# Optimization experiments

Measured on AMD Instinct MI355X. Metric: run time of the kernel, lower is better.

The kernel has to match this reference:

```python
import jax, jax.numpy as jnp
from jax import lax
import numpy as np

T, B, I, U = 512, 64, 512, 512
FORGET_BIAS = 1.0  # matches forget_bias=1.0; cell_clip=None -> no clipping; no peephole


def setup_inputs() -> dict:
    key = jax.random.key(0)
    kx, kw = jax.random.split(key)
    x = jax.random.normal(kx, (T, B, I), dtype=jnp.float32)
    cs0 = jnp.zeros((B, U), dtype=jnp.float32)
    h0 = jnp.zeros((B, U), dtype=jnp.float32)
    # kernel [input_size + num_units, 4*num_units], bias [4*num_units] (zeros init as in build())
    w = jax.random.normal(kw, (I + U, 4 * U), dtype=jnp.float32) * 0.05
    b = jnp.zeros((4 * U,), dtype=jnp.float32)
    return {"x": x, "cs0": cs0, "h0": h0, "w": w, "b": b}


def reference(x, cs0, h0, w, b):
    """Fused BlockLSTM forward. Returns (h_seq [T,B,U], final_cs, final_h),
    mirroring LSTMBlockWrapper.call -> (outputs, (cell_state, output))."""

    def step(carry, x_t):
        cs_prev, h_prev = carry
        z = jnp.concatenate([x_t, h_prev], axis=-1) @ w + b  # [B, 4U]
        # TF BlockLSTM gate order: i, ci (cell input), f, o
        zi, zci, zf, zo = jnp.split(z, 4, axis=-1)
        i = jax.nn.sigmoid(zi)
        f = jax.nn.sigmoid(zf + FORGET_BIAS)
        ci = jnp.tanh(zci)
        cs = ci * i + cs_prev * f  # no cell_clip (cell_clip=-1)
        h = jnp.tanh(cs) * jax.nn.sigmoid(zo)
        return (cs, h), h

    (final_cs, final_h), h_seq = lax.scan(step, (cs0, h0), x)
    return h_seq, final_cs, final_h
```

## Files before the change

kernel.cpp:

```cpp
#include <hip/hip_runtime.h>


#define T_STEPS 512
#define NB 64
#define NU 512
#define NI 512
#define KTOT 1024
#define ZCOLS 2048
#define HSEQ_ELEMS (T_STEPS * NB * NU)
#define POISON64 0x7FC07FC07FC07FC0ull
#define SLEEP_PRE 10

typedef float    floatx4   __attribute__((ext_vector_type(4)));
typedef __bf16   bf16x8    __attribute__((ext_vector_type(8)));
typedef unsigned short ushortx8 __attribute__((ext_vector_type(8)));
typedef unsigned long long ull_t;

static __device__ __forceinline__ unsigned short f2bf(float f) {
  unsigned int u = __builtin_bit_cast(unsigned int, f);
  u += 0x7fffu + ((u >> 16) & 1u);
  return (unsigned short)(u >> 16);
}
static __device__ __forceinline__ float bf2f(unsigned short h) {
  unsigned int u = ((unsigned int)h) << 16;
  return __builtin_bit_cast(float, u);
}
static __device__ __forceinline__ float sigmoidf_(float x) {
  return __builtin_amdgcn_rcpf(1.0f + __expf(-x));
}
static __device__ __forceinline__ float fast_tanhf(float x) {
  const float ax = fabsf(x);
  const float t = __expf(-2.0f * ax);
  const float r = (1.0f - t) * __builtin_amdgcn_rcpf(1.0f + t);
  return copysignf(r, x);
}
static __device__ __forceinline__ bf16x8 ldfrag(const unsigned short* p) {
  ushortx8 v = *reinterpret_cast<const ushortx8*>(p);
  return __builtin_bit_cast(bf16x8, v);
}
static __device__ __forceinline__ ull_t pack4bf(float a, float b, float c, float d) {
  return (ull_t)f2bf(a) | ((ull_t)f2bf(b) << 16) | ((ull_t)f2bf(c) << 32) |
         ((ull_t)f2bf(d) << 48);
}
static __device__ __forceinline__ bf16x8 mkfrag(ull_t lo, ull_t hi) {
  struct P { ull_t a, b; } s{lo, hi};
  return __builtin_bit_cast(bf16x8, s);
}

__global__ __launch_bounds__(256) void init_kernel(const float* __restrict__ h0,
                                                   unsigned short* __restrict__ hbf) {
  const int j = blockIdx.x * 256 + threadIdx.x;
  if (j < 524288) {
    ull_t* p = reinterpret_cast<ull_t*>(&hbf[32768 + (size_t)j * 32]);
#pragma unroll
    for (int r = 0; r < 8; ++r) p[r] = POISON64;
  } else {
    const int k = j - 524288;
#pragma unroll
    for (int p2 = 0; p2 < 2; ++p2) {
      const int i = k * 2 + p2;
      const int row = i >> 6, chunk = i & 63;
      const float* src = &h0[row * NU + chunk * 8];
      const ull_t lo = pack4bf(src[0], src[4], src[1], src[5]);
      const ull_t hi = pack4bf(src[2], src[6], src[3], src[7]);
      const size_t off =
          (size_t)(chunk >> 2) * 2048 + (size_t)(chunk & 3) * 512 + (size_t)row * 8;
      *reinterpret_cast<ull_t*>(&hbf[off]) = lo;
      *reinterpret_cast<ull_t*>(&hbf[off + 4]) = hi;
    }
  }
}

__global__ __launch_bounds__(256) void transpose_w_kernel(
    const float* __restrict__ w, unsigned short* __restrict__ wT) {
  __shared__ float tile[32][33];
  const int u0 = blockIdx.x * 32;
  const int k0 = blockIdx.y * 32;
  const int g = blockIdx.z;
  const int tx = threadIdx.x & 31, ty = threadIdx.x >> 5;
#pragma unroll
  for (int r = 0; r < 4; ++r) {
    const int k = ty + r * 8;
    tile[k][tx] = w[(size_t)(k0 + k) * ZCOLS + g * 512 + u0 + tx];
  }
  __syncthreads();
#pragma unroll
  for (int r = 0; r < 4; ++r) {
    const int u = ty + r * 8;
    const int kk = k0 + tx;
    int kd = kk;
    if (kk >= 512) {
      const int u3 = kk & 7;
      kd = (kk & ~7) | (((u3 & 3) << 1) | (u3 >> 2));
    }
    wT[(size_t)((u0 + u) * 4 + g) * KTOT + kd] = f2bf(tile[tx][u]);
  }
}

__global__ __launch_bounds__(256) void gemm_zx_kernel(
    const float* __restrict__ x, const unsigned short* __restrict__ wT,
    const float* __restrict__ bias, unsigned short* __restrict__ zxp) {
  __shared__ __align__(16) unsigned short As[128][32];
  __shared__ __align__(16) unsigned short Bs[128][32];
  const int m0 = blockIdx.y * 128;
  const int n0 = blockIdx.x * 128;
  const int tid = threadIdx.x;
  const int wid = tid >> 6, lane = tid & 63;
  const int quad = lane >> 4, nl = lane & 15;
  const int wm = (wid & 1) * 64, wn = (wid >> 1) * 64;
  const int srow = tid >> 3;
  const int skk = (tid & 7) * 4;

  floatx4 acc[4][4] = {};

  for (int kt = 0; kt < 16; ++kt) {
    const int k0 = kt * 32;
    __syncthreads();
#pragma unroll
    for (int r = 0; r < 4; ++r) {
      const int row = r * 32 + srow;
      const float4 v =
          *reinterpret_cast<const float4*>(&x[(size_t)(m0 + row) * NI + k0 + skk]);
      *reinterpret_cast<ull_t*>(&As[row][skk]) = pack4bf(v.x, v.y, v.z, v.w);
      *reinterpret_cast<ull_t*>(&Bs[row][skk]) =
          *reinterpret_cast<const ull_t*>(&wT[(size_t)(n0 + row) * KTOT + k0 + skk]);
    }
    __syncthreads();
    bf16x8 af[4], bfr[4];
#pragma unroll
    for (int i = 0; i < 4; ++i) {
      af[i] = ldfrag(&As[wm + i * 16 + nl][quad * 8]);
      bfr[i] = ldfrag(&Bs[wn + i * 16 + nl][quad * 8]);
    }
#pragma unroll
    for (int i = 0; i < 4; ++i)
#pragma unroll
      for (int j = 0; j < 4; ++j)
        acc[i][j] =
            __builtin_amdgcn_mfma_f32_16x16x32_bf16(af[i], bfr[j], acc[i][j], 0, 0, 0);
  }

  float bv[4];
#pragma unroll
  for (int j = 0; j < 4; ++j) {
    const int colp = n0 + wn + j * 16 + nl;
    bv[j] = bias[(colp & 3) * 512 + (colp >> 2)];
  }
#pragma unroll
  for (int i = 0; i < 4; ++i) {
    const int browb = wm + i * 16 + quad * 4;
    const int t = (m0 + browb) >> 6;
    const int rt = (browb >> 5) & 1;
    const int hi = (browb & 31) >> 3;
    const int qb = (browb >> 2) & 1;
#pragma unroll
    for (int j = 0; j < 4; ++j) {
      const int colp = n0 + wn + j * 16 + nl;
      const int cbl = colp >> 5;
      const int lanep = (colp & 31) + 32 * qb;
      const ull_t packed =
          pack4bf(acc[i][j][0] + bv[j], acc[i][j][1] + bv[j],
                  acc[i][j][2] + bv[j], acc[i][j][3] + bv[j]);
      *reinterpret_cast<ull_t*>(
          &zxp[((((size_t)t * 64 + cbl) * 2 + rt) * 64 + lanep) * 16 + hi * 4]) = packed;
    }
  }
}

__global__ __launch_bounds__(64) void lstm_rec_kernel(
    const unsigned short* __restrict__ zxp, const unsigned short* __restrict__ wT,
    const float* __restrict__ cs_init, float* __restrict__ out,
    unsigned short* __restrict__ hbf) {
  const int lane = threadIdx.x;
  const int bid = blockIdx.x;
  const int cb = bid >> 2;
  const int qr = bid & 3;
  const int l15 = lane & 15, quad = lane >> 4;
  const int row = qr * 16 + l15;

  bf16x8 Wf[2][16];
#pragma unroll
  for (int cf = 0; cf < 2; ++cf)
#pragma unroll
    for (int kf = 0; kf < 16; ++kf)
      Wf[cf][kf] = ldfrag(
          &wT[(size_t)(cb * 32 + cf * 16 + l15) * KTOT + 512 + kf * 32 + quad * 8]);

  float csv[2];
  csv[0] = cs_init[row * NU + cb * 8 + quad];
  csv[1] = cs_init[row * NU + cb * 8 + 4 + quad];

  ull_t AL[16], AH[16];
  auto issueA = [&](int tt) {
    const unsigned short* p0 =
        hbf + (size_t)tt * 32768 + (size_t)quad * 512 + (size_t)row * 8;
#pragma unroll
    for (int kf = 0; kf < 16; ++kf) {
      const unsigned short* p = p0 + (size_t)kf * 2048;
      AL[kf] = __hip_atomic_load((const ull_t*)p, __ATOMIC_RELAXED,
                                 __HIP_MEMORY_SCOPE_AGENT);
      AH[kf] = __hip_atomic_load((const ull_t*)(p + 4), __ATOMIC_RELAXED,
                                 __HIP_MEMORY_SCOPE_AGENT);
    }
  };

  unsigned short zxv[8];
  const int rt_ = qr >> 1;
  const int qb_ = (l15 >> 2) & 1;
  const int hi_ = (qr & 1) * 2 + (l15 >> 3);
  const int rr_ = l15 & 3;
  auto issueZ = [&](int tt) {
    const size_t base = (((size_t)tt * 64 + cb) * 2 + rt_) * 64;
#pragma unroll
    for (int cf = 0; cf < 2; ++cf)
#pragma unroll
      for (int g = 0; g < 4; ++g) {
        const int c5 = cf * 16 + quad * 4 + g;
        zxv[cf * 4 + g] = zxp[(base + (size_t)(c5 + 32 * qb_)) * 16 + hi_ * 4 + rr_];
      }
  };

  issueA(0);
  issueZ(0);

  for (int t = 0; t < T_STEPS; ++t) {
    floatx4 z0, z1;
    int tries = 0;
    while (true) {
      floatx4 p00 = {0.f, 0.f, 0.f, 0.f}, p01 = {0.f, 0.f, 0.f, 0.f};
      floatx4 p10 = {0.f, 0.f, 0.f, 0.f}, p11 = {0.f, 0.f, 0.f, 0.f};
#pragma unroll
      for (int kf = 0; kf < 8; ++kf) {
        const bf16x8 hlo = mkfrag(AL[kf], AH[kf]);
        const bf16x8 hhi = mkfrag(AL[8 + kf], AH[8 + kf]);
        p00 = __builtin_amdgcn_mfma_f32_16x16x32_bf16(Wf[0][kf], hlo, p00, 0, 0, 0);
        p01 = __builtin_amdgcn_mfma_f32_16x16x32_bf16(Wf[1][kf], hlo, p01, 0, 0, 0);
        p10 = __builtin_amdgcn_mfma_f32_16x16x32_bf16(Wf[0][8 + kf], hhi, p10, 0, 0, 0);
        p11 = __builtin_amdgcn_mfma_f32_16x16x32_bf16(Wf[1][8 + kf], hhi, p11, 0, 0, 0);
      }
      z0 = p00 + p10;
      z1 = p01 + p11;
      const float s = ((z0[0] + z0[1]) + (z0[2] + z0[3])) +
                      ((z1[0] + z1[1]) + (z1[2] + z1[3]));
      if (!__any(s != s) || ++tries >= (1 << 16)) break;
      issueA(t);
    }

    float hout[2];
    {
      const float iv = sigmoidf_(z0[0] + bf2f(zxv[0]));
      const float civ = fast_tanhf(z0[1] + bf2f(zxv[1]));
      const float fv = sigmoidf_(z0[2] + bf2f(zxv[2]) + 1.0f);
      const float ov = sigmoidf_(z0[3] + bf2f(zxv[3]));
      csv[0] = civ * iv + csv[0] * fv;
      hout[0] = fast_tanhf(csv[0]) * ov;
    }
    {
      const float iv = sigmoidf_(z1[0] + bf2f(zxv[4]));
      const float civ = fast_tanhf(z1[1] + bf2f(zxv[5]));
      const float fv = sigmoidf_(z1[2] + bf2f(zxv[6]) + 1.0f);
      const float ov = sigmoidf_(z1[3] + bf2f(zxv[7]));
      csv[1] = civ * iv + csv[1] * fv;
      hout[1] = fast_tanhf(csv[1]) * ov;
    }

    const unsigned hv = (unsigned)f2bf(hout[0]) | ((unsigned)f2bf(hout[1]) << 16);
    unsigned short* hw = &hbf[(size_t)(t + 1) * 32768 + (size_t)(cb >> 2) * 2048 +
                              (size_t)(cb & 3) * 512 + (size_t)row * 8 + 2 * quad];
    __hip_atomic_store(reinterpret_cast<unsigned*>(hw), hv, __ATOMIC_RELAXED,
                       __HIP_MEMORY_SCOPE_AGENT);
    asm volatile("" ::: "memory");

    float* op = &out[((size_t)t * NB + row) * NU + cb * 8];
    op[quad] = hout[0];
    op[4 + quad] = hout[1];
    if (t == T_STEPS - 1) {
      float* cp = &out[HSEQ_ELEMS + (size_t)row * NU + cb * 8];
      cp[quad] = csv[0];
      cp[4 + quad] = csv[1];
      float* hp2 = &out[HSEQ_ELEMS + NB * NU + (size_t)row * NU + cb * 8];
      hp2[quad] = hout[0];
      hp2[4 + quad] = hout[1];
    }

    if (t + 1 < T_STEPS) {
      __builtin_amdgcn_s_sleep(SLEEP_PRE);
      asm volatile("" ::: "memory");
      issueA(t + 1);
      issueZ(t + 1);
    }
  }
}

extern "C" void kernel_launch(void* const* d_in, const int* in_sizes, int n_in,
                              void* d_out, int out_size, void* d_ws, size_t ws_size,
                              hipStream_t stream) {
  const float* x = (const float*)d_in[0];
  const float* cs0 = (const float*)d_in[1];
  const float* h0 = (const float*)d_in[2];
  const float* w = (const float*)d_in[3];
  const float* bias = (const float*)d_in[4];
  float* out = (float*)d_out;

  char* ws = (char*)d_ws;
  unsigned short* wT = (unsigned short*)(ws);
  unsigned short* zxp = (unsigned short*)(ws + (size_t)(4 << 20));
  unsigned short* hbf = (unsigned short*)(ws + (size_t)(132 << 20));

  init_kernel<<<dim3(2056), 256, 0, stream>>>(h0, hbf);
  transpose_w_kernel<<<dim3(16, 32, 4), 256, 0, stream>>>(w, wT);
  gemm_zx_kernel<<<dim3(16, 256), 256, 0, stream>>>(x, wT, bias, zxp);
  lstm_rec_kernel<<<dim3(256), 64, 0, stream>>>(zxp, wT, cs0, out, hbf);
}
```

Baseline: 1.315 ms.

## Partition recurrent LSTM by XCD with per-XCD batch groups and coherence-tuned polling

The persistent recurrent kernel now assigns work by XCD. Each workgroup reads its hardware XCC id and claims a slot from a per-XCD atomic counter, so every 8-row batch group is handled entirely within one XCD. Extra workgroups exit early. The h buffer layout is reorganised per 8-row group, so polling loads can use non-agent-scope (L2-local) dwordx4 loads, with a fallback to system-coherent loads when a group is not native or keeps retrying. It also removes the fixed sleep, double-buffers the zx prefetch, and overlaps the zx load with compute. The risks are that half the MFMA rows are wasted, the kernel relies on XCD placement from launching 1024 blocks, and correctness depends on cache coherence behaviour.

```diff
diff --git a/kernel.cpp b/kernel.cpp
--- a/kernel.cpp
+++ b/kernel.cpp
@@ -9,7 +9,6 @@
 #define ZCOLS 2048
 #define HSEQ_ELEMS (T_STEPS * NB * NU)
 #define POISON64 0x7FC07FC07FC07FC0ull
-#define SLEEP_PRE 10
 
 typedef float    floatx4   __attribute__((ext_vector_type(4)));
 typedef __bf16   bf16x8    __attribute__((ext_vector_type(8)));
@@ -42,13 +41,11 @@
   return (ull_t)f2bf(a) | ((ull_t)f2bf(b) << 16) | ((ull_t)f2bf(c) << 32) |
          ((ull_t)f2bf(d) << 48);
 }
-static __device__ __forceinline__ bf16x8 mkfrag(ull_t lo, ull_t hi) {
-  struct P { ull_t a, b; } s{lo, hi};
-  return __builtin_bit_cast(bf16x8, s);
-}
 
 __global__ __launch_bounds__(256) void init_kernel(const float* __restrict__ h0,
-                                                   unsigned short* __restrict__ hbf) {
+                                                   unsigned short* __restrict__ hbf,
+                                                   unsigned int* __restrict__ qcnt) {
+  if (blockIdx.x == 0 && threadIdx.x < 8) qcnt[threadIdx.x * 64] = 0;
   const int j = blockIdx.x * 256 + threadIdx.x;
   if (j < 524288) {
     ull_t* p = reinterpret_cast<ull_t*>(&hbf[32768 + (size_t)j * 32]);
@@ -59,12 +56,12 @@
 #pragma unroll
     for (int p2 = 0; p2 < 2; ++p2) {
       const int i = k * 2 + p2;
-      const int row = i >> 6, chunk = i & 63;
-      const float* src = &h0[row * NU + chunk * 8];
+      const int row = i >> 6, cb = i & 63;
+      const float* src = &h0[row * NU + cb * 8];
       const ull_t lo = pack4bf(src[0], src[4], src[1], src[5]);
       const ull_t hi = pack4bf(src[2], src[6], src[3], src[7]);
-      const size_t off =
-          (size_t)(chunk >> 2) * 2048 + (size_t)(chunk & 3) * 512 + (size_t)row * 8;
+      const size_t off = (size_t)(row >> 3) * 4096 + (size_t)(cb >> 2) * 256 +
+                         (size_t)(cb & 3) * 64 + (size_t)(row & 7) * 8;
       *reinterpret_cast<ull_t*>(&hbf[off]) = lo;
       *reinterpret_cast<ull_t*>(&hbf[off + 4]) = hi;
     }
@@ -170,13 +167,26 @@
 __global__ __launch_bounds__(64) void lstm_rec_kernel(
     const unsigned short* __restrict__ zxp, const unsigned short* __restrict__ wT,
     const float* __restrict__ cs_init, float* __restrict__ out,
-    unsigned short* __restrict__ hbf) {
+    unsigned short* __restrict__ hbf, unsigned int* __restrict__ qcnt) {
   const int lane = threadIdx.x;
-  const int bid = blockIdx.x;
-  const int cb = bid >> 2;
-  const int qr = bid & 3;
+
+  unsigned xcd;
+  asm volatile("s_getreg_b32 %0, hwreg(HW_REG_XCC_ID)" : "=s"(xcd));
+  xcd &= 7;
+  int g = -1, cb = -1;
+  bool native = false;
+  for (int q = 0; q < 8; ++q) {
+    const int qq = (int)((xcd + q) & 7);
+    int s = 0;
+    if (lane == 0) s = (int)atomicAdd(&qcnt[qq * 64], 1u);
+    s = __shfl(s, 0);
+    if (s < 64) { g = qq; cb = s; native = (q == 0); break; }
+  }
+  if (g < 0) return;
+
   const int l15 = lane & 15, quad = lane >> 4;
-  const int row = qr * 16 + l15;
+  const int r8 = l15 & 7;
+  const int row = g * 8 + r8;
 
   bf16x8 Wf[2][16];
 #pragma unroll
@@ -190,49 +200,59 @@
   csv[0] = cs_init[row * NU + cb * 8 + quad];
   csv[1] = cs_init[row * NU + cb * 8 + 4 + quad];
 
-  ull_t AL[16], AH[16];
-  auto issueA = [&](int tt) {
+  floatx4 Af[16];
+  auto issueA = [&](int tt, bool ag) {
     const unsigned short* p0 =
-        hbf + (size_t)tt * 32768 + (size_t)quad * 512 + (size_t)row * 8;
-#pragma unroll
-    for (int kf = 0; kf < 16; ++kf) {
-      const unsigned short* p = p0 + (size_t)kf * 2048;
-      AL[kf] = __hip_atomic_load((const ull_t*)p, __ATOMIC_RELAXED,
-                                 __HIP_MEMORY_SCOPE_AGENT);
-      AH[kf] = __hip_atomic_load((const ull_t*)(p + 4), __ATOMIC_RELAXED,
-                                 __HIP_MEMORY_SCOPE_AGENT);
+        hbf + (size_t)tt * 32768 + (size_t)g * 4096 + quad * 64 + r8 * 8;
+    if (ag) {
+#pragma unroll
+      for (int kf = 0; kf < 16; ++kf)
+        asm volatile("global_load_dwordx4 %0, %1, off sc0 sc1"
+                     : "=v"(Af[kf]) : "v"(p0 + (size_t)kf * 256) : "memory");
+    } else {
+#pragma unroll
+      for (int kf = 0; kf < 16; ++kf)
+        asm volatile("global_load_dwordx4 %0, %1, off sc0"
+                     : "=v"(Af[kf]) : "v"(p0 + (size_t)kf * 256) : "memory");
     }
   };
 
-  unsigned short zxv[8];
-  const int rt_ = qr >> 1;
-  const int qb_ = (l15 >> 2) & 1;
-  const int hi_ = (qr & 1) * 2 + (l15 >> 3);
-  const int rr_ = l15 & 3;
-  auto issueZ = [&](int tt) {
+  const int rt_ = row >> 5;
+  const int qb_ = (row >> 2) & 1;
+  const int hi_ = (row & 31) >> 3;
+  const int rr_ = row & 3;
+  auto issueZ = [&](int tt, unsigned short (&zb)[8]) {
     const size_t base = (((size_t)tt * 64 + cb) * 2 + rt_) * 64;
 #pragma unroll
     for (int cf = 0; cf < 2; ++cf)
 #pragma unroll
-      for (int g = 0; g < 4; ++g) {
-        const int c5 = cf * 16 + quad * 4 + g;
-        zxv[cf * 4 + g] = zxp[(base + (size_t)(c5 + 32 * qb_)) * 16 + hi_ * 4 + rr_];
+      for (int gg = 0; gg < 4; ++gg) {
+        const int c5 = cf * 16 + quad * 4 + gg;
+        zb[cf * 4 + gg] = zxp[(base + (size_t)(c5 + 32 * qb_)) * 16 + hi_ * 4 + rr_];
       }
   };
 
-  issueA(0);
-  issueZ(0);
-
-  for (int t = 0; t < T_STEPS; ++t) {
+  unsigned short zA[8], zB[8];
+  bool agent = !native;
+  int astreak = 0;
+
+  issueA(0, agent);
+  issueZ(0, zA);
+  asm volatile("" ::: "memory");
+
+  auto step = [&](int t, unsigned short (&zrd)[8], unsigned short (&zwr)[8]) {
     floatx4 z0, z1;
     int tries = 0;
-    while (true) {
+    bool sa = agent;
+    for (;;) {
+      asm volatile("s_waitcnt vmcnt(0)" ::: "memory");
+      __builtin_amdgcn_sched_barrier(0);
       floatx4 p00 = {0.f, 0.f, 0.f, 0.f}, p01 = {0.f, 0.f, 0.f, 0.f};
       floatx4 p10 = {0.f, 0.f, 0.f, 0.f}, p11 = {0.f, 0.f, 0.f, 0.f};
 #pragma unroll
       for (int kf = 0; kf < 8; ++kf) {
-        const bf16x8 hlo = mkfrag(AL[kf], AH[kf]);
-        const bf16x8 hhi = mkfrag(AL[8 + kf], AH[8 + kf]);
+        const bf16x8 hlo = __builtin_bit_cast(bf16x8, Af[kf]);
+        const bf16x8 hhi = __builtin_bit_cast(bf16x8, Af[8 + kf]);
         p00 = __builtin_amdgcn_mfma_f32_16x16x32_bf16(Wf[0][kf], hlo, p00, 0, 0, 0);
         p01 = __builtin_amdgcn_mfma_f32_16x16x32_bf16(Wf[1][kf], hlo, p01, 0, 0, 0);
         p10 = __builtin_amdgcn_mfma_f32_16x16x32_bf16(Wf[0][8 + kf], hhi, p10, 0, 0, 0);
@@ -243,52 +263,66 @@
       const float s = ((z0[0] + z0[1]) + (z0[2] + z0[3])) +
                       ((z1[0] + z1[1]) + (z1[2] + z1[3]));
       if (!__any(s != s) || ++tries >= (1 << 16)) break;
-      issueA(t);
-    }
+      if (!sa && tries >= 8) sa = true;
+      issueA(t, sa);
+    }
+    if (!agent) {
+      if (sa) { if (++astreak >= 16) agent = true; }
+      else astreak = 0;
+    }
+
+    if (t + 1 < T_STEPS) issueZ(t + 1, zwr);
+    asm volatile("" ::: "memory");
 
     float hout[2];
     {
-      const float iv = sigmoidf_(z0[0] + bf2f(zxv[0]));
-      const float civ = fast_tanhf(z0[1] + bf2f(zxv[1]));
-      const float fv = sigmoidf_(z0[2] + bf2f(zxv[2]) + 1.0f);
-      const float ov = sigmoidf_(z0[3] + bf2f(zxv[3]));
+      const float iv = sigmoidf_(z0[0] + bf2f(zrd[0]));
+      const float civ = fast_tanhf(z0[1] + bf2f(zrd[1]));
+      const float fv = sigmoidf_(z0[2] + bf2f(zrd[2]) + 1.0f);
+      const float ov = sigmoidf_(z0[3] + bf2f(zrd[3]));
       csv[0] = civ * iv + csv[0] * fv;
       hout[0] = fast_tanhf(csv[0]) * ov;
     }
     {
-      const float iv = sigmoidf_(z1[0] + bf2f(zxv[4]));
-      const float civ = fast_tanhf(z1[1] + bf2f(zxv[5]));
-      const float fv = sigmoidf_(z1[2] + bf2f(zxv[6]) + 1.0f);
-      const float ov = sigmoidf_(z1[3] + bf2f(zxv[7]));
+      const float iv = sigmoidf_(z1[0] + bf2f(zrd[4]));
+      const float civ = fast_tanhf(z1[1] + bf2f(zrd[5]));
+      const float fv = sigmoidf_(z1[2] + bf2f(zrd[6]) + 1.0f);
+      const float ov = sigmoidf_(z1[3] + bf2f(zrd[7]));
       csv[1] = civ * iv + csv[1] * fv;
       hout[1] = fast_tanhf(csv[1]) * ov;
     }
 
     const unsigned hv = (unsigned)f2bf(hout[0]) | ((unsigned)f2bf(hout[1]) << 16);
-    unsigned short* hw = &hbf[(size_t)(t + 1) * 32768 + (size_t)(cb >> 2) * 2048 +
-                              (size_t)(cb & 3) * 512 + (size_t)row * 8 + 2 * quad];
-    __hip_atomic_store(reinterpret_cast<unsigned*>(hw), hv, __ATOMIC_RELAXED,
-                       __HIP_MEMORY_SCOPE_AGENT);
+    if (l15 < 8) {
+      unsigned short* hw = &hbf[(size_t)(t + 1) * 32768 + (size_t)g * 4096 +
+                                (size_t)(cb >> 2) * 256 + (size_t)(cb & 3) * 64 +
+                                (size_t)r8 * 8 + 2 * quad];
+      __hip_atomic_store(reinterpret_cast<unsigned*>(hw), hv, __ATOMIC_RELAXED,
+                         __HIP_MEMORY_SCOPE_AGENT);
+    }
     asm volatile("" ::: "memory");
 
-    float* op = &out[((size_t)t * NB + row) * NU + cb * 8];
-    op[quad] = hout[0];
-    op[4 + quad] = hout[1];
-    if (t == T_STEPS - 1) {
-      float* cp = &out[HSEQ_ELEMS + (size_t)row * NU + cb * 8];
-      cp[quad] = csv[0];
-      cp[4 + quad] = csv[1];
-      float* hp2 = &out[HSEQ_ELEMS + NB * NU + (size_t)row * NU + cb * 8];
-      hp2[quad] = hout[0];
-      hp2[4 + quad] = hout[1];
-    }
-
-    if (t + 1 < T_STEPS) {
-      __builtin_amdgcn_s_sleep(SLEEP_PRE);
-      asm volatile("" ::: "memory");
-      issueA(t + 1);
-      issueZ(t + 1);
-    }
+    if (l15 < 8) {
+      float* op = &out[((size_t)t * NB + row) * NU + cb * 8];
+      op[quad] = hout[0];
+      op[4 + quad] = hout[1];
+      if (t == T_STEPS - 1) {
+        float* cp = &out[HSEQ_ELEMS + (size_t)row * NU + cb * 8];
+        cp[quad] = csv[0];
+        cp[4 + quad] = csv[1];
+        float* hp2 = &out[HSEQ_ELEMS + NB * NU + (size_t)row * NU + cb * 8];
+        hp2[quad] = hout[0];
+        hp2[4 + quad] = hout[1];
+      }
+    }
+    asm volatile("" ::: "memory");
+
+    if (t + 1 < T_STEPS) issueA(t + 1, agent);
+  };
+
+  for (int t = 0; t < T_STEPS; t += 2) {
+    step(t, zA, zB);
+    step(t + 1, zB, zA);
   }
 }
 
@@ -306,9 +340,10 @@
   unsigned short* wT = (unsigned short*)(ws);
   unsigned short* zxp = (unsigned short*)(ws + (size_t)(4 << 20));
   unsigned short* hbf = (unsigned short*)(ws + (size_t)(132 << 20));
-
-  init_kernel<<<dim3(2056), 256, 0, stream>>>(h0, hbf);
+  unsigned int* qcnt = (unsigned int*)(ws + (size_t)(164 << 20) + (1 << 16));
+
+  init_kernel<<<dim3(2056), 256, 0, stream>>>(h0, hbf, qcnt);
   transpose_w_kernel<<<dim3(16, 32, 4), 256, 0, stream>>>(w, wT);
   gemm_zx_kernel<<<dim3(16, 256), 256, 0, stream>>>(x, wT, bias, zxp);
-  lstm_rec_kernel<<<dim3(256), 64, 0, stream>>>(zxp, wT, cs0, out, hbf);
-}
+  lstm_rec_kernel<<<dim3(1024), 64, 0, stream>>>(zxp, wT, cs0, out, hbf, qcnt);
+}
```

Measured after the change: 2.448 ms. +86.2%, slower.
